# Optimization experiments

Measured on AMD Instinct MI355X. Metric: run time of the kernel, lower is better.

## Reference

```python
import jax, jax.numpy as jnp
import numpy as np

B, N, E = 8, 5000, 100000
IN_DIM, OUT_DIM = 128, 128
EPS = 1e-5


def setup_inputs() -> dict:
    key = jax.random.key(0)
    ks = jax.random.split(key, 8)
    node_features = jax.random.normal(ks[0], (B, N, IN_DIM), dtype=jnp.float32)
    edge_index = jax.random.randint(ks[1], (B, 2, E), 0, N, dtype=jnp.int32)
    node_mask = jnp.ones((B, N), dtype=jnp.float32)
    edge_mask = jnp.ones((B, E), dtype=jnp.float32)
    s = 1.0 / np.sqrt(IN_DIM)
    W_self = jax.random.uniform(ks[2], (IN_DIM, OUT_DIM), minval=-s, maxval=s, dtype=jnp.float32)
    b_self = jax.random.uniform(ks[3], (OUT_DIM,), minval=-s, maxval=s, dtype=jnp.float32)
    W_nb = jax.random.uniform(ks[4], (IN_DIM, OUT_DIM), minval=-s, maxval=s, dtype=jnp.float32)
    b_nb = jax.random.uniform(ks[5], (OUT_DIM,), minval=-s, maxval=s, dtype=jnp.float32)
    gamma = jnp.ones((OUT_DIM,), dtype=jnp.float32)
    beta = jnp.zeros((OUT_DIM,), dtype=jnp.float32)
    return {"node_features": node_features, "edge_index": edge_index,
            "node_mask": node_mask, "edge_mask": edge_mask,
            "W_self": W_self, "b_self": b_self, "W_nb": W_nb, "b_nb": b_nb,
            "gamma": gamma, "beta": beta}


def _aggregate_mean(x, ei, em):
    # x: [N, D], ei: [2, E], em: [E]. Masked segment-mean over incoming edges.
    src, tgt = ei[0], ei[1]
    sf = x[src] * em[:, None]                                   # [E, D]
    sums = jax.ops.segment_sum(sf, tgt, num_segments=N)         # [N, D]
    cnt = jax.ops.segment_sum(em, tgt, num_segments=N)          # [N]
    return sums / jnp.maximum(cnt, 1.0)[:, None]


def reference(node_features, edge_index, node_mask, edge_mask,
              W_self, b_self, W_nb, b_nb, gamma, beta):
    self_feat = jnp.einsum('bnd,do->bno', node_features, W_self) + b_self
    agg = jax.vmap(_aggregate_mean)(node_features, edge_index, edge_mask)  # [B,N,D]
    nb_feat = jnp.einsum('bnd,do->bno', agg, W_nb) + b_nb
    out = jax.nn.relu(self_feat + nb_feat)
    # dropout in eval mode -> identity
    mu = jnp.mean(out, axis=-1, keepdims=True)
    var = jnp.var(out, axis=-1, keepdims=True)
    out = (out - mu) * jax.lax.rsqrt(var + EPS) * gamma + beta
    return out * node_mask[..., None]
```

## Files before the change

kernel.cpp:

```cpp
#include <hip/hip_runtime.h>


#define B_ 8
#define N_ 5000
#define E_ 100000
#define D_ 128
#define EPS_ 1e-5f
#define NNODES (B_ * N_)
#define NEDGES (B_ * E_)
#define JB 313
#define PPB ((E_ / 2 + 255) / 256)
#define FILL_BLOCKS (8 * PPB)
#define CONV_BLOCKS 2500
#define CAP 64
#define LDSP 136

typedef __bf16 bf16x8 __attribute__((ext_vector_type(8)));
typedef float  f32x4  __attribute__((ext_vector_type(4)));

static __device__ __forceinline__ unsigned short f2bf(float f) {
    union { float f; unsigned int i; } c; c.f = f;
    unsigned int i = c.i;
    i += 0x7fffu + ((i >> 16) & 1u);
    return (unsigned short)(i >> 16);
}
static __device__ __forceinline__ float bflo(unsigned int u) {
    return __uint_as_float(u << 16);
}
static __device__ __forceinline__ float bfhi(unsigned int u) {
    return __uint_as_float(u & 0xffff0000u);
}

__global__ __launch_bounds__(256) void fill_k(
    const int* __restrict__ ei, const float* __restrict__ em,
    int* __restrict__ cnt, unsigned int* __restrict__ entries,
    const float* __restrict__ x, unsigned short* __restrict__ xbf,
    const float* __restrict__ Wself, const float* __restrict__ Wnb,
    unsigned short* __restrict__ Bt)
{
    int blk = blockIdx.x;
    if (blk < FILL_BLOCKS) {
        int b = blk & 7;
        int p = (blk >> 3) * 256 + threadIdx.x;
        if (p >= E_ / 2) return;
        int e = 2 * p;
        const int* eib = ei + (size_t)b * 2 * E_;
        int2   sv = *(const int2*)(eib + e);
        int2   tv = *(const int2*)(eib + E_ + e);
        float2 mv = *(const float2*)(em + (size_t)b * E_ + e);
        int gb = b * N_;
        if (mv.x != 0.0f) {
            int g = gb + tv.x;
            int slot = atomicAdd(&cnt[g], 1);
            if (slot < CAP)
                entries[((size_t)g << 6) + slot] =
                    (unsigned int)(gb + sv.x) | ((unsigned int)f2bf(mv.x) << 16);
        }
        if (mv.y != 0.0f) {
            int g = gb + tv.y;
            int slot = atomicAdd(&cnt[g], 1);
            if (slot < CAP)
                entries[((size_t)g << 6) + slot] =
                    (unsigned int)(gb + sv.y) | ((unsigned int)f2bf(mv.y) << 16);
        }
    } else if (blk < FILL_BLOCKS + CONV_BLOCKS) {
        size_t base = (size_t)(blk - FILL_BLOCKS) * 2048 + threadIdx.x * 8;
        float4 va = *(const float4*)(x + base);
        float4 vb = *(const float4*)(x + base + 4);
        uint4 o;
        o.x = (unsigned int)f2bf(va.x) | ((unsigned int)f2bf(va.y) << 16);
        o.y = (unsigned int)f2bf(va.z) | ((unsigned int)f2bf(va.w) << 16);
        o.z = (unsigned int)f2bf(vb.x) | ((unsigned int)f2bf(vb.y) << 16);
        o.w = (unsigned int)f2bf(vb.z) | ((unsigned int)f2bf(vb.w) << 16);
        *(uint4*)(xbf + base) = o;
    } else {
        int n = blk - FILL_BLOCKS - CONV_BLOCKS;
        int k = threadIdx.x;
        float v = (k < 128) ? Wself[(size_t)k * D_ + n]
                            : Wnb[(size_t)(k - 128) * D_ + n];
        Bt[(size_t)n * 256 + k] = f2bf(v);
    }
}

__global__ __launch_bounds__(256) void fused_k(
    const unsigned short* __restrict__ xbf, const int* __restrict__ cnt,
    const unsigned int* __restrict__ entries,
    const unsigned short* __restrict__ Bt,
    const float* __restrict__ bself, const float* __restrict__ bnb,
    const float* __restrict__ gamma, const float* __restrict__ beta,
    const float* __restrict__ nmask, float* __restrict__ out)
{
    __shared__ unsigned short xs[16][LDSP];
    __shared__ unsigned short as[16][LDSP];
    __shared__ float red[4][2][16];

    int t = threadIdx.x;
    int lane = t & 63, wv = t >> 6;
    int b = blockIdx.x & 7;
    int j = blockIdx.x >> 3;
    int i0 = j * 16;
    int g0 = b * N_ + i0;
    int limit = N_ - i0; if (limit > 16) limit = 16;

    int grp = lane >> 4;
    int c8  = lane & 15;
    int myrow = (wv << 2) + grp;

    int ga = g0 + ((myrow < limit) ? myrow : 0);
    int dgr = cnt[ga];
    unsigned int ee = entries[((size_t)ga << 6) + c8];

    #pragma unroll
    for (int lr = wv * 4; lr < wv * 4 + 4; ++lr) {
        unsigned int v = 0;
        if (lr < limit)
            v = ((const unsigned int*)(xbf + (size_t)(g0 + lr) * D_))[lane];
        ((unsigned int*)&xs[lr][0])[lane] = v;
    }

    int dgg = (myrow < limit) ? ((dgr > CAP) ? CAP : dgr) : 0;

    float a[8];
    #pragma unroll
    for (int i = 0; i < 8; ++i) a[i] = 0.f;
    float cs = 0.f;

    for (int k0 = 0; ; k0 += 16) {
        unsigned int een = 0u;
        if (k0 + 16 < CAP)
            een = entries[((size_t)ga << 6) + (k0 + 16) + c8];
        #pragma unroll 8
        for (int k = 0; k < 16; ++k) {
            unsigned int ej = (unsigned int)__shfl((int)ee, (lane & 48) + k, 64);
            int   ok = (k0 + k) < dgg;
            int   sj = ok ? (int)(ej & 0xffffu) : 0;
            float mj = ok ? __uint_as_float(ej & 0xffff0000u) : 0.0f;
            uint4 v = *(const uint4*)(xbf + (size_t)sj * D_ + (c8 << 3));
            a[0] += bflo(v.x) * mj; a[1] += bfhi(v.x) * mj;
            a[2] += bflo(v.y) * mj; a[3] += bfhi(v.y) * mj;
            a[4] += bflo(v.z) * mj; a[5] += bfhi(v.z) * mj;
            a[6] += bflo(v.w) * mj; a[7] += bfhi(v.w) * mj;
            cs += mj;
        }
        if (k0 + 16 >= CAP) break;
        if (__all(dgg <= k0 + 16)) break;
        ee = een;
    }

    {
        float inv = 1.0f / fmaxf(cs, 1.0f);
        uint4 o;
        o.x = (unsigned int)f2bf(a[0] * inv) | ((unsigned int)f2bf(a[1] * inv) << 16);
        o.y = (unsigned int)f2bf(a[2] * inv) | ((unsigned int)f2bf(a[3] * inv) << 16);
        o.z = (unsigned int)f2bf(a[4] * inv) | ((unsigned int)f2bf(a[5] * inv) << 16);
        o.w = (unsigned int)f2bf(a[6] * inv) | ((unsigned int)f2bf(a[7] * inv) << 16);
        *(uint4*)&as[myrow][c8 << 3] = o;
    }
    __syncthreads();

    int quad = lane >> 4;
    int lcol = lane & 15;

    f32x4 acc[2];
    acc[0] = (f32x4)0.0f;
    acc[1] = (f32x4)0.0f;

    #pragma unroll
    for (int kk = 0; kk < 4; ++kk) {
        int kof = kk * 32 + quad * 8;
        bf16x8 av = *(const bf16x8*)&xs[lcol][kof];
        #pragma unroll
        for (int p = 0; p < 2; ++p) {
            int tt = wv * 2 + p;
            bf16x8 bf = *(const bf16x8*)(Bt + (size_t)(tt * 16 + lcol) * 256 + kof);
            acc[p] = __builtin_amdgcn_mfma_f32_16x16x32_bf16(av, bf, acc[p], 0, 0, 0);
        }
    }
    #pragma unroll
    for (int kk = 0; kk < 4; ++kk) {
        int kof = kk * 32 + quad * 8;
        bf16x8 av = *(const bf16x8*)&as[lcol][kof];
        #pragma unroll
        for (int p = 0; p < 2; ++p) {
            int tt = wv * 2 + p;
            bf16x8 bf = *(const bf16x8*)(Bt + (size_t)(tt * 16 + lcol) * 256 + 128 + kof);
            acc[p] = __builtin_amdgcn_mfma_f32_16x16x32_bf16(av, bf, acc[p], 0, 0, 0);
        }
    }

    float h[2][4];
    float s[4] = {0, 0, 0, 0}, q[4] = {0, 0, 0, 0};
    float gam[2], bet[2];
    #pragma unroll
    for (int p = 0; p < 2; ++p) {
        int col = (wv * 2 + p) * 16 + lcol;
        float bs = bself[col] + bnb[col];
        gam[p] = gamma[col];
        bet[p] = beta[col];
        #pragma unroll
        for (int r = 0; r < 4; ++r) {
            float v = fmaxf(acc[p][r] + bs, 0.0f);
            h[p][r] = v;
            s[r] += v;
            q[r] += v * v;
        }
    }
    #pragma unroll
    for (int r = 0; r < 4; ++r) {
        #pragma unroll
        for (int off = 1; off <= 8; off <<= 1) {
            s[r] += __shfl_xor(s[r], off, 64);
            q[r] += __shfl_xor(q[r], off, 64);
        }
    }
    if (lcol == 0) {
        #pragma unroll
        for (int r = 0; r < 4; ++r) {
            red[wv][0][quad * 4 + r] = s[r];
            red[wv][1][quad * 4 + r] = q[r];
        }
    }
    __syncthreads();

    #pragma unroll
    for (int r = 0; r < 4; ++r) {
        int row = quad * 4 + r;
        int irow = i0 + row;
        if (irow >= N_) continue;
        float S = red[0][0][row] + red[1][0][row] + red[2][0][row] + red[3][0][row];
        float Q = red[0][1][row] + red[1][1][row] + red[2][1][row] + red[3][1][row];
        float mu = S * (1.0f / D_);
        float var = Q * (1.0f / D_) - mu * mu;
        float rin = rsqrtf(fmaxf(var, 0.0f) + EPS_);
        int g = b * N_ + irow;
        float mk = nmask[g];
        float* op = out + (size_t)g * D_;
        #pragma unroll
        for (int p = 0; p < 2; ++p) {
            int col = (wv * 2 + p) * 16 + lcol;
            op[col] = ((h[p][r] - mu) * rin * gam[p] + bet[p]) * mk;
        }
    }
}

extern "C" void kernel_launch(void* const* d_in, const int* in_sizes, int n_in,
                              void* d_out, int out_size, void* d_ws, size_t ws_size,
                              hipStream_t stream)
{
    const float* x     = (const float*)d_in[0];
    const int*   ei    = (const int*)d_in[1];
    const float* nmask = (const float*)d_in[2];
    const float* em    = (const float*)d_in[3];
    const float* Wself = (const float*)d_in[4];
    const float* bself = (const float*)d_in[5];
    const float* Wnb   = (const float*)d_in[6];
    const float* bnb   = (const float*)d_in[7];
    const float* gamma = (const float*)d_in[8];
    const float* beta  = (const float*)d_in[9];
    float* out = (float*)d_out;

    int* cnt = (int*)d_ws;
    unsigned int* entries = (unsigned int*)(cnt + NNODES);
    unsigned short* Bt = (unsigned short*)(entries + (size_t)NNODES * CAP);
    unsigned short* xbf = Bt + (size_t)128 * 256;

    hipMemsetAsync(cnt, 0, NNODES * sizeof(int), stream);
    fill_k<<<FILL_BLOCKS + CONV_BLOCKS + 128, 256, 0, stream>>>(
        ei, em, cnt, entries, x, xbf, Wself, Wnb, Bt);
    fused_k<<<8 * JB, 256, 0, stream>>>(xbf, cnt, entries, Bt,
                                        bself, bnb, gamma, beta, nmask, out);
}
```

Measured before the change: 161.2 us.

## Pad atomic counters to separate cache lines and batch gather loads in chunks of eight

Measured after the change: 165.9 us. 1.03x slower.

```diff
diff --git a/kernel.cpp b/kernel.cpp
--- a/kernel.cpp
+++ b/kernel.cpp
@@ -14,6 +14,7 @@
 #define CONV_BLOCKS 2500
 #define CAP 64
 #define LDSP 136
+#define CPAD 16
 
 typedef __bf16 bf16x8 __attribute__((ext_vector_type(8)));
 typedef float  f32x4  __attribute__((ext_vector_type(4)));
@@ -49,20 +50,16 @@
         int2   tv = *(const int2*)(eib + E_ + e);
         float2 mv = *(const float2*)(em + (size_t)b * E_ + e);
         int gb = b * N_;
-        if (mv.x != 0.0f) {
-            int g = gb + tv.x;
-            int slot = atomicAdd(&cnt[g], 1);
-            if (slot < CAP)
-                entries[((size_t)g << 6) + slot] =
-                    (unsigned int)(gb + sv.x) | ((unsigned int)f2bf(mv.x) << 16);
-        }
-        if (mv.y != 0.0f) {
-            int g = gb + tv.y;
-            int slot = atomicAdd(&cnt[g], 1);
-            if (slot < CAP)
-                entries[((size_t)g << 6) + slot] =
-                    (unsigned int)(gb + sv.y) | ((unsigned int)f2bf(mv.y) << 16);
-        }
+        int g0 = gb + tv.x, g1 = gb + tv.y;
+        int e0 = (mv.x != 0.0f), e1 = (mv.y != 0.0f);
+        int s0 = atomicAdd(&cnt[g0 * CPAD], e0);
+        int s1 = atomicAdd(&cnt[g1 * CPAD], e1);
+        if (e0 && s0 < CAP)
+            entries[((size_t)g0 << 6) + s0] =
+                (unsigned int)(gb + sv.x) | ((unsigned int)f2bf(mv.x) << 16);
+        if (e1 && s1 < CAP)
+            entries[((size_t)g1 << 6) + s1] =
+                (unsigned int)(gb + sv.y) | ((unsigned int)f2bf(mv.y) << 16);
     } else if (blk < FILL_BLOCKS + CONV_BLOCKS) {
         size_t base = (size_t)(blk - FILL_BLOCKS) * 2048 + threadIdx.x * 8;
         float4 va = *(const float4*)(x + base);
@@ -82,6 +79,30 @@
     }
 }
 
+#define GCHUNK(EE, OFS, SB)                                                   \
+  {                                                                           \
+    unsigned int ej[8]; float mj[8]; uint4 v[8];                              \
+    _Pragma("unroll")                                                         \
+    for (int k = 0; k < 8; ++k)                                               \
+      ej[k] = (unsigned int)__shfl((int)(EE), lanebase + (OFS) + k, 64);      \
+    _Pragma("unroll")                                                         \
+    for (int k = 0; k < 8; ++k) {                                             \
+      int ok = (SB) + k < dgg;                                                \
+      int sj = ok ? (int)(ej[k] & 0xffffu) : 0;                               \
+      mj[k] = ok ? __uint_as_float(ej[k] & 0xffff0000u) : 0.0f;               \
+      v[k] = *(const uint4*)(xbf + ((size_t)sj << 7) + (c8 << 3));            \
+    }                                                                         \
+    _Pragma("unroll")                                                         \
+    for (int k = 0; k < 8; ++k) {                                             \
+      float m = mj[k];                                                        \
+      a[0] += bflo(v[k].x) * m; a[1] += bfhi(v[k].x) * m;                     \
+      a[2] += bflo(v[k].y) * m; a[3] += bfhi(v[k].y) * m;                     \
+      a[4] += bflo(v[k].z) * m; a[5] += bfhi(v[k].z) * m;                     \
+      a[6] += bflo(v[k].w) * m; a[7] += bfhi(v[k].w) * m;                     \
+      cs += m;                                                                \
+    }                                                                         \
+  }
+
 __global__ __launch_bounds__(256) void fused_k(
     const unsigned short* __restrict__ xbf, const int* __restrict__ cnt,
     const unsigned int* __restrict__ entries,
@@ -104,11 +125,14 @@
 
     int grp = lane >> 4;
     int c8  = lane & 15;
+    int lanebase = lane & 48;
     int myrow = (wv << 2) + grp;
 
     int ga = g0 + ((myrow < limit) ? myrow : 0);
-    int dgr = cnt[ga];
-    unsigned int ee = entries[((size_t)ga << 6) + c8];
+    int dgr = cnt[ga * CPAD];
+    const unsigned int* ep = entries + ((size_t)ga << 6);
+    unsigned int ee0 = ep[c8];
+    unsigned int ee1 = ep[16 + c8];
 
     #pragma unroll
     for (int lr = wv * 4; lr < wv * 4 + 4; ++lr) {
@@ -125,26 +149,17 @@
     for (int i = 0; i < 8; ++i) a[i] = 0.f;
     float cs = 0.f;
 
-    for (int k0 = 0; ; k0 += 16) {
-        unsigned int een = 0u;
-        if (k0 + 16 < CAP)
-            een = entries[((size_t)ga << 6) + (k0 + 16) + c8];
-        #pragma unroll 8
-        for (int k = 0; k < 16; ++k) {
-            unsigned int ej = (unsigned int)__shfl((int)ee, (lane & 48) + k, 64);
-            int   ok = (k0 + k) < dgg;
-            int   sj = ok ? (int)(ej & 0xffffu) : 0;
-            float mj = ok ? __uint_as_float(ej & 0xffff0000u) : 0.0f;
-            uint4 v = *(const uint4*)(xbf + (size_t)sj * D_ + (c8 << 3));
-            a[0] += bflo(v.x) * mj; a[1] += bfhi(v.x) * mj;
-            a[2] += bflo(v.y) * mj; a[3] += bfhi(v.y) * mj;
-            a[4] += bflo(v.z) * mj; a[5] += bfhi(v.z) * mj;
-            a[6] += bflo(v.w) * mj; a[7] += bfhi(v.w) * mj;
-            cs += mj;
-        }
-        if (k0 + 16 >= CAP) break;
-        if (__all(dgg <= k0 + 16)) break;
-        ee = een;
+    if (0 < dgg)  GCHUNK(ee0, 0, 0);
+    if (8 < dgg)  GCHUNK(ee0, 8, 8);
+    if (16 < dgg) GCHUNK(ee1, 0, 16);
+    if (24 < dgg) GCHUNK(ee1, 8, 24);
+    if (__any(dgg > 32)) {
+        #pragma unroll 1
+        for (int c = 4; c < 8; ++c) {
+            unsigned int ee = ep[(c << 3) + (c8 & 7)];
+            if ((c << 3) < dgg) GCHUNK(ee, 0, c << 3);
+            if (__all(dgg <= ((c + 1) << 3))) break;
+        }
     }
 
     {
@@ -260,11 +275,11 @@
     float* out = (float*)d_out;
 
     int* cnt = (int*)d_ws;
-    unsigned int* entries = (unsigned int*)(cnt + NNODES);
+    unsigned int* entries = (unsigned int*)(cnt + (size_t)NNODES * CPAD);
     unsigned short* Bt = (unsigned short*)(entries + (size_t)NNODES * CAP);
     unsigned short* xbf = Bt + (size_t)128 * 256;
 
-    hipMemsetAsync(cnt, 0, NNODES * sizeof(int), stream);
+    hipMemsetAsync(cnt, 0, (size_t)NNODES * CPAD * sizeof(int), stream);
     fill_k<<<FILL_BLOCKS + CONV_BLOCKS + 128, 256, 0, stream>>>(
         ei, em, cnt, entries, x, xbf, Wself, Wnb, Bt);
     fused_k<<<8 * JB, 256, 0, stream>>>(xbf, cnt, entries, Bt,
```

## Split fused gather+GEMM into separate wave-per-node gather and GEMM kernels

Applied to the files above, without the earlier changes.

Result: slower. 171.9 us (+6.6%).

```diff
diff --git a/kernel.cpp b/kernel.cpp
--- a/kernel.cpp
+++ b/kernel.cpp
@@ -14,6 +14,7 @@
 #define CONV_BLOCKS 2500
 #define CAP 64
 #define LDSP 136
+#define GATHER_BLOCKS (NNODES / 4)
 
 typedef __bf16 bf16x8 __attribute__((ext_vector_type(8)));
 typedef float  f32x4  __attribute__((ext_vector_type(4)));
@@ -49,20 +50,16 @@
         int2   tv = *(const int2*)(eib + E_ + e);
         float2 mv = *(const float2*)(em + (size_t)b * E_ + e);
         int gb = b * N_;
-        if (mv.x != 0.0f) {
-            int g = gb + tv.x;
-            int slot = atomicAdd(&cnt[g], 1);
-            if (slot < CAP)
-                entries[((size_t)g << 6) + slot] =
-                    (unsigned int)(gb + sv.x) | ((unsigned int)f2bf(mv.x) << 16);
-        }
-        if (mv.y != 0.0f) {
-            int g = gb + tv.y;
-            int slot = atomicAdd(&cnt[g], 1);
-            if (slot < CAP)
-                entries[((size_t)g << 6) + slot] =
-                    (unsigned int)(gb + sv.y) | ((unsigned int)f2bf(mv.y) << 16);
-        }
+        int g0 = gb + tv.x, g1 = gb + tv.y;
+        int e0 = (mv.x != 0.0f), e1 = (mv.y != 0.0f);
+        int s0 = atomicAdd(&cnt[g0], e0);
+        int s1 = atomicAdd(&cnt[g1], e1);
+        if (e0 && s0 < CAP)
+            entries[((size_t)g0 << 6) + s0] =
+                (unsigned int)(gb + sv.x) | ((unsigned int)f2bf(mv.x) << 16);
+        if (e1 && s1 < CAP)
+            entries[((size_t)g1 << 6) + s1] =
+                (unsigned int)(gb + sv.y) | ((unsigned int)f2bf(mv.y) << 16);
     } else if (blk < FILL_BLOCKS + CONV_BLOCKS) {
         size_t base = (size_t)(blk - FILL_BLOCKS) * 2048 + threadIdx.x * 8;
         float4 va = *(const float4*)(x + base);
@@ -82,9 +79,83 @@
     }
 }
 
-__global__ __launch_bounds__(256) void fused_k(
+__global__ __launch_bounds__(256) void gather_k(
     const unsigned short* __restrict__ xbf, const int* __restrict__ cnt,
-    const unsigned int* __restrict__ entries,
+    const unsigned int* __restrict__ entries, unsigned short* __restrict__ aggbf)
+{
+    int t = threadIdx.x;
+    int lane = t & 63, wv = t >> 6;
+    int g = (blockIdx.x & 7) * N_ + (blockIdx.x >> 3) * 4 + wv;
+
+    int sq = lane >> 4;
+    int c8 = lane & 15;
+
+    int dg = cnt[g]; if (dg > CAP) dg = CAP;
+    unsigned int ee = entries[((size_t)g << 6) + lane];
+
+    float a[8];
+    #pragma unroll
+    for (int i = 0; i < 8; ++i) a[i] = 0.f;
+    float cs = 0.f;
+
+    uint4 v[8]; float mj[8];
+    #pragma unroll
+    for (int q = 0; q < 8; ++q) {
+        unsigned int ej = (unsigned int)__shfl((int)ee, 4 * q + sq, 64);
+        int ok = 4 * q + sq < dg;
+        int sj = ok ? (int)(ej & 0xffffu) : 0;
+        mj[q] = ok ? __uint_as_float(ej & 0xffff0000u) : 0.0f;
+        v[q] = *(const uint4*)(xbf + ((size_t)sj << 7) + (c8 << 3));
+    }
+    #pragma unroll
+    for (int q = 0; q < 8; ++q) {
+        if (4 * q < dg) {
+            float m = mj[q];
+            a[0] += bflo(v[q].x) * m; a[1] += bfhi(v[q].x) * m;
+            a[2] += bflo(v[q].y) * m; a[3] += bfhi(v[q].y) * m;
+            a[4] += bflo(v[q].z) * m; a[5] += bfhi(v[q].z) * m;
+            a[6] += bflo(v[q].w) * m; a[7] += bfhi(v[q].w) * m;
+            cs += m;
+        }
+    }
+    if (dg > 32) {
+        #pragma unroll 1
+        for (int q = 8; q < 16; ++q) {
+            if (4 * q >= dg) break;
+            unsigned int ej = (unsigned int)__shfl((int)ee, 4 * q + sq, 64);
+            int ok = 4 * q + sq < dg;
+            int sj = ok ? (int)(ej & 0xffffu) : 0;
+            float m = ok ? __uint_as_float(ej & 0xffff0000u) : 0.0f;
+            uint4 w = *(const uint4*)(xbf + ((size_t)sj << 7) + (c8 << 3));
+            a[0] += bflo(w.x) * m; a[1] += bfhi(w.x) * m;
+            a[2] += bflo(w.y) * m; a[3] += bfhi(w.y) * m;
+            a[4] += bflo(w.z) * m; a[5] += bfhi(w.z) * m;
+            a[6] += bflo(w.w) * m; a[7] += bfhi(w.w) * m;
+            cs += m;
+        }
+    }
+
+    #pragma unroll
+    for (int i = 0; i < 8; ++i) {
+        a[i] += __shfl_xor(a[i], 16, 64);
+        a[i] += __shfl_xor(a[i], 32, 64);
+    }
+    cs += __shfl_xor(cs, 16, 64);
+    cs += __shfl_xor(cs, 32, 64);
+
+    if (lane < 16) {
+        float inv = 1.0f / fmaxf(cs, 1.0f);
+        uint4 o;
+        o.x = (unsigned int)f2bf(a[0] * inv) | ((unsigned int)f2bf(a[1] * inv) << 16);
+        o.y = (unsigned int)f2bf(a[2] * inv) | ((unsigned int)f2bf(a[3] * inv) << 16);
+        o.z = (unsigned int)f2bf(a[4] * inv) | ((unsigned int)f2bf(a[5] * inv) << 16);
+        o.w = (unsigned int)f2bf(a[6] * inv) | ((unsigned int)f2bf(a[7] * inv) << 16);
+        *(uint4*)(aggbf + ((size_t)g << 7) + (c8 << 3)) = o;
+    }
+}
+
+__global__ __launch_bounds__(256) void gemm_k(
+    const unsigned short* __restrict__ xbf, const unsigned short* __restrict__ aggbf,
     const unsigned short* __restrict__ Bt,
     const float* __restrict__ bself, const float* __restrict__ bnb,
     const float* __restrict__ gamma, const float* __restrict__ beta,
@@ -102,59 +173,15 @@
     int g0 = b * N_ + i0;
     int limit = N_ - i0; if (limit > 16) limit = 16;
 
-    int grp = lane >> 4;
-    int c8  = lane & 15;
-    int myrow = (wv << 2) + grp;
-
-    int ga = g0 + ((myrow < limit) ? myrow : 0);
-    int dgr = cnt[ga];
-    unsigned int ee = entries[((size_t)ga << 6) + c8];
-
     #pragma unroll
     for (int lr = wv * 4; lr < wv * 4 + 4; ++lr) {
-        unsigned int v = 0;
-        if (lr < limit)
-            v = ((const unsigned int*)(xbf + (size_t)(g0 + lr) * D_))[lane];
-        ((unsigned int*)&xs[lr][0])[lane] = v;
-    }
-
-    int dgg = (myrow < limit) ? ((dgr > CAP) ? CAP : dgr) : 0;
-
-    float a[8];
-    #pragma unroll
-    for (int i = 0; i < 8; ++i) a[i] = 0.f;
-    float cs = 0.f;
-
-    for (int k0 = 0; ; k0 += 16) {
-        unsigned int een = 0u;
-        if (k0 + 16 < CAP)
-            een = entries[((size_t)ga << 6) + (k0 + 16) + c8];
-        #pragma unroll 8
-        for (int k = 0; k < 16; ++k) {
-            unsigned int ej = (unsigned int)__shfl((int)ee, (lane & 48) + k, 64);
-            int   ok = (k0 + k) < dgg;
-            int   sj = ok ? (int)(ej & 0xffffu) : 0;
-            float mj = ok ? __uint_as_float(ej & 0xffff0000u) : 0.0f;
-            uint4 v = *(const uint4*)(xbf + (size_t)sj * D_ + (c8 << 3));
-            a[0] += bflo(v.x) * mj; a[1] += bfhi(v.x) * mj;
-            a[2] += bflo(v.y) * mj; a[3] += bfhi(v.y) * mj;
-            a[4] += bflo(v.z) * mj; a[5] += bfhi(v.z) * mj;
-            a[6] += bflo(v.w) * mj; a[7] += bfhi(v.w) * mj;
-            cs += mj;
-        }
-        if (k0 + 16 >= CAP) break;
-        if (__all(dgg <= k0 + 16)) break;
-        ee = een;
-    }
-
-    {
-        float inv = 1.0f / fmaxf(cs, 1.0f);
-        uint4 o;
-        o.x = (unsigned int)f2bf(a[0] * inv) | ((unsigned int)f2bf(a[1] * inv) << 16);
-        o.y = (unsigned int)f2bf(a[2] * inv) | ((unsigned int)f2bf(a[3] * inv) << 16);
-        o.z = (unsigned int)f2bf(a[4] * inv) | ((unsigned int)f2bf(a[5] * inv) << 16);
-        o.w = (unsigned int)f2bf(a[6] * inv) | ((unsigned int)f2bf(a[7] * inv) << 16);
-        *(uint4*)&as[myrow][c8 << 3] = o;
+        unsigned int vx = 0, va = 0;
+        if (lr < limit) {
+            vx = ((const unsigned int*)(xbf + (size_t)(g0 + lr) * D_))[lane];
+            va = ((const unsigned int*)(aggbf + (size_t)(g0 + lr) * D_))[lane];
+        }
+        ((unsigned int*)&xs[lr][0])[lane] = vx;
+        ((unsigned int*)&as[lr][0])[lane] = va;
     }
     __syncthreads();
 
@@ -263,10 +290,12 @@
     unsigned int* entries = (unsigned int*)(cnt + NNODES);
     unsigned short* Bt = (unsigned short*)(entries + (size_t)NNODES * CAP);
     unsigned short* xbf = Bt + (size_t)128 * 256;
+    unsigned short* aggbf = xbf + (size_t)NNODES * D_;
 
     hipMemsetAsync(cnt, 0, NNODES * sizeof(int), stream);
     fill_k<<<FILL_BLOCKS + CONV_BLOCKS + 128, 256, 0, stream>>>(
         ei, em, cnt, entries, x, xbf, Wself, Wnb, Bt);
-    fused_k<<<8 * JB, 256, 0, stream>>>(xbf, cnt, entries, Bt,
-                                        bself, bnb, gamma, beta, nmask, out);
-}
+    gather_k<<<GATHER_BLOCKS, 256, 0, stream>>>(xbf, cnt, entries, aggbf);
+    gemm_k<<<8 * JB, 256, 0, stream>>>(xbf, aggbf, Bt,
+                                       bself, bnb, gamma, beta, nmask, out);
+}
```
